# Kernel optimization log

Measured on AMD Instinct MI355X. Metric: run time of the kernel, lower is better.

The kernel has to match this reference:

```python
import jax, jax.numpy as jnp
import numpy as np

DIM = 1024
NUM_HEADS = 16
HEAD_DIM = DIM // NUM_HEADS
SCALE = HEAD_DIM ** -0.5


def setup_inputs() -> dict:
    key = jax.random.key(0)
    ks = jax.random.split(key, 13)
    B, Tq, Tk = 2, 1024, 4096
    s = DIM ** -0.5  # nn.Linear-like init scale
    inp = {
        'query': jax.random.normal(ks[0], (B, Tq, DIM), jnp.float32),
        'key': jax.random.normal(ks[1], (B, Tk, DIM), jnp.float32),
        'value': jax.random.normal(ks[2], (B, Tk, DIM), jnp.float32),
        'Wq': jax.random.normal(ks[3], (DIM, DIM), jnp.float32) * s,
        'bq': jnp.zeros((DIM,), jnp.float32),
        'Wk': jax.random.normal(ks[4], (DIM, DIM), jnp.float32) * s,
        'bk': jnp.zeros((DIM,), jnp.float32),
        'Wv': jax.random.normal(ks[5], (DIM, DIM), jnp.float32) * s,
        'bv': jnp.zeros((DIM,), jnp.float32),
        'Wo': jax.random.normal(ks[6], (DIM, DIM), jnp.float32) * s,
        'bo': jnp.zeros((DIM,), jnp.float32),
        'ln_gamma': jnp.ones((DIM,), jnp.float32),
        'ln_beta': jnp.zeros((DIM,), jnp.float32),
    }
    return inp


def _layer_norm(x, gamma, beta, eps=1e-5):
    mu = jnp.mean(x, axis=-1, keepdims=True)
    var = jnp.var(x, axis=-1, keepdims=True)
    return (x - mu) * jax.lax.rsqrt(var + eps) * gamma + beta


def reference(query, key, value, Wq, bq, Wk, bk, Wv, bv, Wo, bo, ln_gamma, ln_beta):
    B, Tq, D = query.shape
    Tk = key.shape[1]
    H, Hd = NUM_HEADS, HEAD_DIM
    # projections -> [B, H, T, Hd]
    q = (query @ Wq.T + bq).reshape(B, Tq, H, Hd).transpose(0, 2, 1, 3)
    k = (key @ Wk.T + bk).reshape(B, Tk, H, Hd).transpose(0, 2, 1, 3)
    v = (value @ Wv.T + bv).reshape(B, Tk, H, Hd).transpose(0, 2, 1, 3)
    scores = jnp.einsum('bhqd,bhkd->bhqk', q, k) * SCALE
    attn = jax.nn.softmax(scores, axis=-1)  # dropout is identity in eval
    out = jnp.einsum('bhqk,bhkd->bhqd', attn, v)
    out = out.transpose(0, 2, 1, 3).reshape(B, Tq, D)
    out = out @ Wo.T + bo
    out = _layer_norm(query + out, ln_gamma, ln_beta)
    return out, attn
```

## Files before the change

### kernel.cpp

```cpp
#include <hip/hip_runtime.h>
#include <hip/hip_bf16.h>

#define BATCH 2
#define TQ 1024
#define TK 4096
#define DIMSZ 1024
#define NH 16
#define HD 64
#define SCALE 0.125f

typedef __bf16 bf16x8 __attribute__((ext_vector_type(8)));
typedef float f32x4 __attribute__((ext_vector_type(4)));

static __device__ inline unsigned short f2bf(float x) {
  union { __bf16 h; unsigned short u; } v;
  v.h = (__bf16)x;
  return v.u;
}
static __device__ inline unsigned int pack2(float a, float b) {
  return (unsigned int)f2bf(a) | ((unsigned int)f2bf(b) << 16);
}

__global__ __launch_bounds__(256) void cast_all(
    const float* __restrict__ q, const float* __restrict__ k,
    const float* __restrict__ v, const float* __restrict__ wq,
    const float* __restrict__ wk, const float* __restrict__ wv,
    const float* __restrict__ wo, unsigned short* __restrict__ qo,
    unsigned short* __restrict__ ko, unsigned short* __restrict__ vo,
    unsigned short* __restrict__ wqo, unsigned short* __restrict__ wko,
    unsigned short* __restrict__ wvo, unsigned short* __restrict__ woo) {
  const float* src;
  unsigned short* dst;
  long n;
  switch (blockIdx.y) {
    case 0: src = q;  dst = qo;  n = (long)BATCH * TQ * DIMSZ; break;
    case 1: src = k;  dst = ko;  n = (long)BATCH * TK * DIMSZ; break;
    case 2: src = v;  dst = vo;  n = (long)BATCH * TK * DIMSZ; break;
    case 3: src = wq; dst = wqo; n = (long)DIMSZ * DIMSZ; break;
    case 4: src = wk; dst = wko; n = (long)DIMSZ * DIMSZ; break;
    case 5: src = wv; dst = wvo; n = (long)DIMSZ * DIMSZ; break;
    default: src = wo; dst = woo; n = (long)DIMSZ * DIMSZ; break;
  }
  const long stride = (long)gridDim.x * 256 * 8;
  for (long i = ((long)blockIdx.x * 256 + threadIdx.x) * 8; i < n; i += stride) {
    const float4 a = *(const float4*)&src[i];
    const float4 b = *(const float4*)&src[i + 4];
    uint4 o;
    o.x = pack2(a.x, a.y);
    o.y = pack2(a.z, a.w);
    o.z = pack2(b.x, b.y);
    o.w = pack2(b.z, b.w);
    *(uint4*)&dst[i] = o;
  }
}

template <bool OUT_BF16>
__global__ __launch_bounds__(256) void gemm_nt(
    const unsigned short* __restrict__ A, const unsigned short* __restrict__ B,
    const float* __restrict__ bias, void* __restrict__ Cout,
    int M, int N, int K) {
  __shared__ unsigned short As[128][40];
  __shared__ unsigned short Bs[128][40];
  const int t = threadIdx.x;
  const int lane = t & 63, wid = t >> 6;
  const int wm = wid >> 1, wn = wid & 1;
  const int l15 = lane & 15, l4 = lane >> 4;
  const int row0 = blockIdx.y * 128, col0 = blockIdx.x * 128;

  f32x4 acc[4][4];
#pragma unroll
  for (int i = 0; i < 4; i++)
#pragma unroll
    for (int j = 0; j < 4; j++) acc[i][j] = (f32x4){0.f, 0.f, 0.f, 0.f};

  for (int k0 = 0; k0 < K; k0 += 32) {
#pragma unroll
    for (int p = 0; p < 2; p++) {
      const int c = t + p * 256;
      const int r = c >> 2, kc = c & 3;
      *(uint4*)&As[r][kc * 8] =
          *(const uint4*)&A[(size_t)(row0 + r) * K + k0 + kc * 8];
      *(uint4*)&Bs[r][kc * 8] =
          *(const uint4*)&B[(size_t)(col0 + r) * K + k0 + kc * 8];
    }
    __syncthreads();
    bf16x8 av[4], bv[4];
#pragma unroll
    for (int f = 0; f < 4; f++) {
      av[f] = *(const bf16x8*)&As[wm * 64 + f * 16 + l15][l4 * 8];
      bv[f] = *(const bf16x8*)&Bs[wn * 64 + f * 16 + l15][l4 * 8];
    }
#pragma unroll
    for (int fm = 0; fm < 4; fm++)
#pragma unroll
      for (int fn = 0; fn < 4; fn++)
        acc[fm][fn] = __builtin_amdgcn_mfma_f32_16x16x32_bf16(
            av[fm], bv[fn], acc[fm][fn], 0, 0, 0);
    __syncthreads();
  }

#pragma unroll
  for (int fm = 0; fm < 4; fm++) {
#pragma unroll
    for (int i = 0; i < 4; i++) {
      const int rr = row0 + wm * 64 + fm * 16 + l4 * 4 + i;
#pragma unroll
      for (int fn = 0; fn < 4; fn++) {
        const int c = col0 + wn * 64 + fn * 16 + l15;
        const float val = acc[fm][fn][i] + bias[c];
        if (OUT_BF16)
          ((unsigned short*)Cout)[(size_t)rr * N + c] = f2bf(val);
        else
          ((float*)Cout)[(size_t)rr * N + c] = val;
      }
    }
  }
}

__global__ __launch_bounds__(256) void transpose_v(
    const unsigned short* __restrict__ vb, unsigned short* __restrict__ vT) {
  const int z = blockIdx.z, b = z >> 4, h = z & 15;
  const int k0 = blockIdx.x * 64;
  __shared__ unsigned short Ts[64][68];
  const int t = threadIdx.x;
  const int c4 = (t & 15) * 4, r = t >> 4;
#pragma unroll
  for (int p = 0; p < 4; p++) {
    const int rr = r + p * 16;
    *(uint2*)&Ts[rr][c4] =
        *(const uint2*)&vb[(size_t)(b * TK + k0 + rr) * DIMSZ + h * HD + c4];
  }
  __syncthreads();
#pragma unroll
  for (int p = 0; p < 4; p++) {
    const int c2 = t + p * 256;
    const int d = c2 >> 4, k4 = (c2 & 15) * 4;
    uint2 o;
    o.x = (unsigned int)Ts[k4][d] | ((unsigned int)Ts[k4 + 1][d] << 16);
    o.y = (unsigned int)Ts[k4 + 2][d] | ((unsigned int)Ts[k4 + 3][d] << 16);
    *(uint2*)&vT[(size_t)(z * HD + d) * TK + k0 + k4] = o;
  }
}

__global__ __launch_bounds__(256) void attn_fused(
    const unsigned short* __restrict__ qb, const unsigned short* __restrict__ kb,
    const unsigned short* __restrict__ vT, float* __restrict__ attn,
    unsigned short* __restrict__ aout) {
  const int dsp = blockIdx.x;
  const int orig = (dsp & 7) * 64 + (dsp >> 3);
  const int z = orig >> 4, mb = orig & 15;
  const int b = z >> 4, h = z & 15;
  const int m0 = mb * 64;

  __shared__ unsigned short Qs[64][72];
  __shared__ unsigned short Ks[128][72];
  __shared__ unsigned short Vs[64][140];
  __shared__ float Pf[64][132];
  __shared__ float partial[64][2];
  __shared__ float rinv[64];

  const int t = threadIdx.x;
  const int lane = t & 63, wid = t >> 6;
  const int wm = wid >> 1, wn = wid & 1;
  const int l15 = lane & 15, l4 = lane >> 4;

#pragma unroll
  for (int p = 0; p < 2; p++) {
    const int idx = t + p * 256;
    const int r = idx >> 3, kc = idx & 7;
    *(uint4*)&Qs[r][kc * 8] =
        *(const uint4*)&qb[(size_t)(b * TQ + m0 + r) * DIMSZ + h * HD + kc * 8];
  }
  __syncthreads();
  bf16x8 aq[2][2];
#pragma unroll
  for (int fm = 0; fm < 2; fm++)
#pragma unroll
    for (int ks = 0; ks < 2; ks++)
      aq[fm][ks] = *(const bf16x8*)&Qs[wm * 32 + fm * 16 + l15][ks * 32 + l4 * 8];

  float rsum[8];
#pragma unroll
  for (int r = 0; r < 8; r++) rsum[r] = 0.f;

  for (int kt = 0; kt < TK / 128; kt++) {
    __syncthreads();
#pragma unroll
    for (int p = 0; p < 4; p++) {
      const int idx = t + p * 256;
      const int r = idx >> 3, kc = idx & 7;
      *(uint4*)&Ks[r][kc * 8] = *(const uint4*)&kb[
          (size_t)(b * TK + kt * 128 + r) * DIMSZ + h * HD + kc * 8];
    }
    __syncthreads();
    bf16x8 bk_[4][2];
#pragma unroll
    for (int fn = 0; fn < 4; fn++)
#pragma unroll
      for (int ks = 0; ks < 2; ks++)
        bk_[fn][ks] =
            *(const bf16x8*)&Ks[wn * 64 + fn * 16 + l15][ks * 32 + l4 * 8];
    f32x4 acc_s[2][4];
#pragma unroll
    for (int i = 0; i < 2; i++)
#pragma unroll
      for (int j = 0; j < 4; j++) acc_s[i][j] = (f32x4){0.f, 0.f, 0.f, 0.f};
#pragma unroll
    for (int ks = 0; ks < 2; ks++)
#pragma unroll
      for (int fm = 0; fm < 2; fm++)
#pragma unroll
        for (int fn = 0; fn < 4; fn++)
          acc_s[fm][fn] = __builtin_amdgcn_mfma_f32_16x16x32_bf16(
              aq[fm][ks], bk_[fn][ks], acc_s[fm][fn], 0, 0, 0);
#pragma unroll
    for (int fm = 0; fm < 2; fm++)
#pragma unroll
      for (int i = 0; i < 4; i++) {
        float s = 0.f;
#pragma unroll
        for (int fn = 0; fn < 4; fn++) s += __expf(acc_s[fm][fn][i] * SCALE);
        rsum[fm * 4 + i] += s;
      }
  }
#pragma unroll
  for (int off = 1; off < 16; off <<= 1)
#pragma unroll
    for (int r = 0; r < 8; r++) rsum[r] += __shfl_xor(rsum[r], off);
  if (l15 == 0) {
#pragma unroll
    for (int fm = 0; fm < 2; fm++)
#pragma unroll
      for (int i = 0; i < 4; i++)
        partial[wm * 32 + fm * 16 + l4 * 4 + i][wn] = rsum[fm * 4 + i];
  }
  __syncthreads();
  if (t < 64) rinv[t] = 1.f / (partial[t][0] + partial[t][1]);

  f32x4 acc_o[4];
#pragma unroll
  for (int j = 0; j < 4; j++) acc_o[j] = (f32x4){0.f, 0.f, 0.f, 0.f};

  float* attn_z = attn + (size_t)z * TQ * TK;

  for (int kt = 0; kt < TK / 128; kt++) {
    __syncthreads();
#pragma unroll
    for (int p = 0; p < 4; p++) {
      const int idx = t + p * 256;
      const int r = idx >> 3, kc = idx & 7;
      *(uint4*)&Ks[r][kc * 8] = *(const uint4*)&kb[
          (size_t)(b * TK + kt * 128 + r) * DIMSZ + h * HD + kc * 8];
    }
#pragma unroll
    for (int p = 0; p < 4; p++) {
      const int idx = t + p * 256;
      const int d = idx >> 4, kc = idx & 15;
      *(uint4*)&Vs[d][kc * 8] =
          *(const uint4*)&vT[(size_t)(z * HD + d) * TK + kt * 128 + kc * 8];
    }
    __syncthreads();

    bf16x8 bk_[4][2];
#pragma unroll
    for (int fn = 0; fn < 4; fn++)
#pragma unroll
      for (int ks = 0; ks < 2; ks++)
        bk_[fn][ks] =
            *(const bf16x8*)&Ks[wn * 64 + fn * 16 + l15][ks * 32 + l4 * 8];
    f32x4 acc_s[2][4];
#pragma unroll
    for (int i = 0; i < 2; i++)
#pragma unroll
      for (int j = 0; j < 4; j++) acc_s[i][j] = (f32x4){0.f, 0.f, 0.f, 0.f};
#pragma unroll
    for (int ks = 0; ks < 2; ks++)
#pragma unroll
      for (int fm = 0; fm < 2; fm++)
#pragma unroll
        for (int fn = 0; fn < 4; fn++)
          acc_s[fm][fn] = __builtin_amdgcn_mfma_f32_16x16x32_bf16(
              aq[fm][ks], bk_[fn][ks], acc_s[fm][fn], 0, 0, 0);

#pragma unroll
    for (int fm = 0; fm < 2; fm++)
#pragma unroll
      for (int i = 0; i < 4; i++) {
        const int row = wm * 32 + fm * 16 + l4 * 4 + i;
        const float iv = rinv[row];
#pragma unroll
        for (int fn = 0; fn < 4; fn++) {
          const int col = wn * 64 + fn * 16 + l15;
          Pf[row][col] = __expf(acc_s[fm][fn][i] * SCALE) * iv;
        }
      }
    __syncthreads();

#pragma unroll
    for (int it = 0; it < 8; it++) {
      const int idx = t + it * 256;
      const int row = idx >> 5, c4 = idx & 31;
      const f32x4 v = *(const f32x4*)&Pf[row][c4 * 4];
      __builtin_nontemporal_store(
          v, (f32x4*)&attn_z[(size_t)(m0 + row) * TK + kt * 128 + c4 * 4]);
    }

#pragma unroll
    for (int ks2 = 0; ks2 < 4; ks2++) {
      const float* pr = &Pf[wid * 16 + l15][ks2 * 32 + l4 * 8];
      const float4 a0 = *(const float4*)pr;
      const float4 a1 = *(const float4*)(pr + 4);
      uint4 pk;
      pk.x = pack2(a0.x, a0.y);
      pk.y = pack2(a0.z, a0.w);
      pk.z = pack2(a1.x, a1.y);
      pk.w = pack2(a1.z, a1.w);
      const bf16x8 ap = *(const bf16x8*)&pk;
#pragma unroll
      for (int fn = 0; fn < 4; fn++) {
        const bf16x8 bvv =
            *(const bf16x8*)&Vs[fn * 16 + l15][ks2 * 32 + l4 * 8];
        acc_o[fn] = __builtin_amdgcn_mfma_f32_16x16x32_bf16(ap, bvv,
                                                            acc_o[fn], 0, 0, 0);
      }
    }
  }

#pragma unroll
  for (int fn = 0; fn < 4; fn++)
#pragma unroll
    for (int i = 0; i < 4; i++) {
      const int rr = m0 + wid * 16 + l4 * 4 + i;
      aout[(size_t)(b * TQ + rr) * DIMSZ + h * HD + fn * 16 + l15] =
          f2bf(acc_o[fn][i]);
    }
}

__global__ __launch_bounds__(256) void residual_ln(
    const float* __restrict__ q, const float* __restrict__ y,
    const float* __restrict__ gamma, const float* __restrict__ beta,
    float* __restrict__ out) {
  __shared__ float w1[4];
  __shared__ float w2[4];
  const size_t base = (size_t)blockIdx.x * DIMSZ;
  const int t = threadIdx.x;

  float x[4];
  float s = 0.f;
#pragma unroll
  for (int i = 0; i < 4; i++) {
    const int c = t + i * 256;
    x[i] = q[base + c] + y[base + c];
    s += x[i];
  }
#pragma unroll
  for (int off = 32; off; off >>= 1) s += __shfl_xor(s, off);
  if ((t & 63) == 0) w1[t >> 6] = s;
  __syncthreads();
  const float mean = (w1[0] + w1[1] + w1[2] + w1[3]) * (1.f / DIMSZ);

  float vs = 0.f;
#pragma unroll
  for (int i = 0; i < 4; i++) {
    const float d = x[i] - mean;
    vs += d * d;
  }
#pragma unroll
  for (int off = 32; off; off >>= 1) vs += __shfl_xor(vs, off);
  if ((t & 63) == 0) w2[t >> 6] = vs;
  __syncthreads();
  const float var = (w2[0] + w2[1] + w2[2] + w2[3]) * (1.f / DIMSZ);
  const float rstd = rsqrtf(var + 1e-5f);

#pragma unroll
  for (int i = 0; i < 4; i++) {
    const int c = t + i * 256;
    out[base + c] = (x[i] - mean) * rstd * gamma[c] + beta[c];
  }
}

extern "C" void kernel_launch(void* const* d_in, const int* in_sizes, int n_in,
                              void* d_out, int out_size, void* d_ws,
                              size_t ws_size, hipStream_t stream) {
  const float* query = (const float*)d_in[0];
  const float* key   = (const float*)d_in[1];
  const float* value = (const float*)d_in[2];
  const float* Wq = (const float*)d_in[3];
  const float* bq = (const float*)d_in[4];
  const float* Wk = (const float*)d_in[5];
  const float* bk = (const float*)d_in[6];
  const float* Wv = (const float*)d_in[7];
  const float* bv = (const float*)d_in[8];
  const float* Wo = (const float*)d_in[9];
  const float* bo = (const float*)d_in[10];
  const float* ln_gamma = (const float*)d_in[11];
  const float* ln_beta  = (const float*)d_in[12];

  float* out  = (float*)d_out;
  float* attn = out + (size_t)BATCH * TQ * DIMSZ;

  const size_t MQ = (size_t)BATCH * TQ * DIMSZ;
  const size_t MK = (size_t)BATCH * TK * DIMSZ;
  const size_t MM = (size_t)DIMSZ * DIMSZ;

  unsigned short* ws = (unsigned short*)d_ws;
  unsigned short* qbf = ws;
  unsigned short* kbf = qbf + MQ;
  unsigned short* vbf = kbf + MK;
  unsigned short* wqb = vbf + MK;
  unsigned short* wkb = wqb + MM;
  unsigned short* wvb = wkb + MM;
  unsigned short* wob = wvb + MM;
  unsigned short* qb  = wob + MM;
  unsigned short* kb  = qb + MQ;
  unsigned short* ab  = kb + MK;
  float* ybuf = (float*)(ab + MQ);

  unsigned short* vbp = kbf;
  unsigned short* vT  = vbf;

  const dim3 blk(256);

  cast_all<<<dim3(1024, 7), blk, 0, stream>>>(query, key, value, Wq, Wk, Wv,
                                              Wo, qbf, kbf, vbf, wqb, wkb,
                                              wvb, wob);

  gemm_nt<true><<<dim3(DIMSZ / 128, (BATCH * TQ) / 128), blk, 0, stream>>>(
      qbf, wqb, bq, qb, BATCH * TQ, DIMSZ, DIMSZ);
  gemm_nt<true><<<dim3(DIMSZ / 128, (BATCH * TK) / 128), blk, 0, stream>>>(
      kbf, wkb, bk, kb, BATCH * TK, DIMSZ, DIMSZ);
  gemm_nt<true><<<dim3(DIMSZ / 128, (BATCH * TK) / 128), blk, 0, stream>>>(
      vbf, wvb, bv, vbp, BATCH * TK, DIMSZ, DIMSZ);

  transpose_v<<<dim3(TK / 64, 1, BATCH * NH), blk, 0, stream>>>(vbp, vT);

  attn_fused<<<dim3(512), blk, 0, stream>>>(qb, kb, vT, attn, ab);

  gemm_nt<false><<<dim3(DIMSZ / 128, (BATCH * TQ) / 128), blk, 0, stream>>>(
      ab, wob, bo, ybuf, BATCH * TQ, DIMSZ, DIMSZ);

  residual_ln<<<dim3(BATCH * TQ), blk, 0, stream>>>(query, ybuf, ln_gamma,
                                                    ln_beta, out);
}
```

Baseline: 369.0 us.

## Halve attention query tile to 32 rows and double grid for occupancy

```diff
diff --git a/kernel.cpp b/kernel.cpp
--- a/kernel.cpp
+++ b/kernel.cpp
@@ -142,172 +142,139 @@
   }
 }
 
-__global__ __launch_bounds__(256) void attn_fused(
+__global__ __launch_bounds__(256, 4) void attn_fused(
     const unsigned short* __restrict__ qb, const unsigned short* __restrict__ kb,
     const unsigned short* __restrict__ vT, float* __restrict__ attn,
     unsigned short* __restrict__ aout) {
   const int dsp = blockIdx.x;
-  const int orig = (dsp & 7) * 64 + (dsp >> 3);
-  const int z = orig >> 4, mb = orig & 15;
+  const int orig = (dsp & 7) * 128 + (dsp >> 3);
+  const int z = orig >> 5, mb = orig & 31;
   const int b = z >> 4, h = z & 15;
-  const int m0 = mb * 64;
-
-  __shared__ unsigned short Qs[64][72];
-  __shared__ unsigned short Ks[128][72];
-  __shared__ unsigned short Vs[64][140];
-  __shared__ float Pf[64][132];
-  __shared__ float partial[64][2];
-  __shared__ float rinv[64];
+  const int m0 = mb * 32;
+
+  __shared__ unsigned short Qs[32][72];
+  __shared__ unsigned short Ks[64][72];
+  __shared__ unsigned short Vs[64][72];
+  __shared__ float Pf[32][68];
+  __shared__ float partial[32][2];
+  __shared__ float rinv[32];
 
   const int t = threadIdx.x;
   const int lane = t & 63, wid = t >> 6;
   const int wm = wid >> 1, wn = wid & 1;
   const int l15 = lane & 15, l4 = lane >> 4;
 
-#pragma unroll
-  for (int p = 0; p < 2; p++) {
-    const int idx = t + p * 256;
-    const int r = idx >> 3, kc = idx & 7;
+  const unsigned short* kb_z = kb + (size_t)b * TK * DIMSZ + h * HD;
+  const unsigned short* vT_z = vT + (size_t)z * HD * TK;
+
+  {
+    const int r = t >> 3, kc = t & 7;
     *(uint4*)&Qs[r][kc * 8] =
         *(const uint4*)&qb[(size_t)(b * TQ + m0 + r) * DIMSZ + h * HD + kc * 8];
   }
   __syncthreads();
-  bf16x8 aq[2][2];
-#pragma unroll
-  for (int fm = 0; fm < 2; fm++)
+  bf16x8 aq[2];
+#pragma unroll
+  for (int ks = 0; ks < 2; ks++)
+    aq[ks] = *(const bf16x8*)&Qs[wm * 16 + l15][ks * 32 + l4 * 8];
+
+  float rsum[4] = {0.f, 0.f, 0.f, 0.f};
+  for (int kt = 0; kt < TK / 64; kt++) {
+    bf16x8 bk_[2][2];
+#pragma unroll
+    for (int fn = 0; fn < 2; fn++)
+#pragma unroll
+      for (int ks = 0; ks < 2; ks++)
+        bk_[fn][ks] = *(const bf16x8*)&kb_z[
+            (size_t)(kt * 64 + wn * 32 + fn * 16 + l15) * DIMSZ + ks * 32 +
+            l4 * 8];
+    f32x4 acc_s[2];
+#pragma unroll
+    for (int j = 0; j < 2; j++) acc_s[j] = (f32x4){0.f, 0.f, 0.f, 0.f};
 #pragma unroll
     for (int ks = 0; ks < 2; ks++)
-      aq[fm][ks] = *(const bf16x8*)&Qs[wm * 32 + fm * 16 + l15][ks * 32 + l4 * 8];
-
-  float rsum[8];
-#pragma unroll
-  for (int r = 0; r < 8; r++) rsum[r] = 0.f;
-
-  for (int kt = 0; kt < TK / 128; kt++) {
+#pragma unroll
+      for (int fn = 0; fn < 2; fn++)
+        acc_s[fn] = __builtin_amdgcn_mfma_f32_16x16x32_bf16(
+            aq[ks], bk_[fn][ks], acc_s[fn], 0, 0, 0);
+#pragma unroll
+    for (int i = 0; i < 4; i++)
+      rsum[i] += __expf(acc_s[0][i] * SCALE) + __expf(acc_s[1][i] * SCALE);
+  }
+#pragma unroll
+  for (int off = 1; off < 16; off <<= 1)
+#pragma unroll
+    for (int i = 0; i < 4; i++) rsum[i] += __shfl_xor(rsum[i], off);
+  if (l15 == 0) {
+#pragma unroll
+    for (int i = 0; i < 4; i++)
+      partial[wm * 16 + l4 * 4 + i][wn] = rsum[i];
+  }
+  __syncthreads();
+  if (t < 32) rinv[t] = 1.f / (partial[t][0] + partial[t][1]);
+  __syncthreads();
+  float riv[4];
+#pragma unroll
+  for (int i = 0; i < 4; i++) riv[i] = rinv[wm * 16 + l4 * 4 + i];
+
+  f32x4 acc_o[2];
+#pragma unroll
+  for (int j = 0; j < 2; j++) acc_o[j] = (f32x4){0.f, 0.f, 0.f, 0.f};
+
+  float* attn_z = attn + (size_t)z * TQ * TK;
+
+  for (int kt = 0; kt < TK / 64; kt++) {
     __syncthreads();
 #pragma unroll
-    for (int p = 0; p < 4; p++) {
+    for (int p = 0; p < 2; p++) {
       const int idx = t + p * 256;
       const int r = idx >> 3, kc = idx & 7;
-      *(uint4*)&Ks[r][kc * 8] = *(const uint4*)&kb[
-          (size_t)(b * TK + kt * 128 + r) * DIMSZ + h * HD + kc * 8];
+      *(uint4*)&Ks[r][kc * 8] =
+          *(const uint4*)&kb_z[(size_t)(kt * 64 + r) * DIMSZ + kc * 8];
+      *(uint4*)&Vs[r][kc * 8] =
+          *(const uint4*)&vT_z[(size_t)r * TK + kt * 64 + kc * 8];
     }
     __syncthreads();
-    bf16x8 bk_[4][2];
-#pragma unroll
-    for (int fn = 0; fn < 4; fn++)
+
+    bf16x8 bk_[2][2];
+#pragma unroll
+    for (int fn = 0; fn < 2; fn++)
 #pragma unroll
       for (int ks = 0; ks < 2; ks++)
         bk_[fn][ks] =
-            *(const bf16x8*)&Ks[wn * 64 + fn * 16 + l15][ks * 32 + l4 * 8];
-    f32x4 acc_s[2][4];
-#pragma unroll
-    for (int i = 0; i < 2; i++)
-#pragma unroll
-      for (int j = 0; j < 4; j++) acc_s[i][j] = (f32x4){0.f, 0.f, 0.f, 0.f};
+            *(const bf16x8*)&Ks[wn * 32 + fn * 16 + l15][ks * 32 + l4 * 8];
+    f32x4 acc_s[2];
+#pragma unroll
+    for (int j = 0; j < 2; j++) acc_s[j] = (f32x4){0.f, 0.f, 0.f, 0.f};
 #pragma unroll
     for (int ks = 0; ks < 2; ks++)
 #pragma unroll
-      for (int fm = 0; fm < 2; fm++)
-#pragma unroll
-        for (int fn = 0; fn < 4; fn++)
-          acc_s[fm][fn] = __builtin_amdgcn_mfma_f32_16x16x32_bf16(
-              aq[fm][ks], bk_[fn][ks], acc_s[fm][fn], 0, 0, 0);
-#pragma unroll
-    for (int fm = 0; fm < 2; fm++)
+      for (int fn = 0; fn < 2; fn++)
+        acc_s[fn] = __builtin_amdgcn_mfma_f32_16x16x32_bf16(
+            aq[ks], bk_[fn][ks], acc_s[fn], 0, 0, 0);
+
+#pragma unroll
+    for (int fn = 0; fn < 2; fn++)
 #pragma unroll
       for (int i = 0; i < 4; i++) {
-        float s = 0.f;
-#pragma unroll
-        for (int fn = 0; fn < 4; fn++) s += __expf(acc_s[fm][fn][i] * SCALE);
-        rsum[fm * 4 + i] += s;
-      }
-  }
-#pragma unroll
-  for (int off = 1; off < 16; off <<= 1)
-#pragma unroll
-    for (int r = 0; r < 8; r++) rsum[r] += __shfl_xor(rsum[r], off);
-  if (l15 == 0) {
-#pragma unroll
-    for (int fm = 0; fm < 2; fm++)
-#pragma unroll
-      for (int i = 0; i < 4; i++)
-        partial[wm * 32 + fm * 16 + l4 * 4 + i][wn] = rsum[fm * 4 + i];
-  }
-  __syncthreads();
-  if (t < 64) rinv[t] = 1.f / (partial[t][0] + partial[t][1]);
-
-  f32x4 acc_o[4];
-#pragma unroll
-  for (int j = 0; j < 4; j++) acc_o[j] = (f32x4){0.f, 0.f, 0.f, 0.f};
-
-  float* attn_z = attn + (size_t)z * TQ * TK;
-
-  for (int kt = 0; kt < TK / 128; kt++) {
-    __syncthreads();
-#pragma unroll
-    for (int p = 0; p < 4; p++) {
-      const int idx = t + p * 256;
-      const int r = idx >> 3, kc = idx & 7;
-      *(uint4*)&Ks[r][kc * 8] = *(const uint4*)&kb[
-          (size_t)(b * TK + kt * 128 + r) * DIMSZ + h * HD + kc * 8];
-    }
-#pragma unroll
-    for (int p = 0; p < 4; p++) {
-      const int idx = t + p * 256;
-      const int d = idx >> 4, kc = idx & 15;
-      *(uint4*)&Vs[d][kc * 8] =
-          *(const uint4*)&vT[(size_t)(z * HD + d) * TK + kt * 128 + kc * 8];
-    }
-    __syncthreads();
-
-    bf16x8 bk_[4][2];
-#pragma unroll
-    for (int fn = 0; fn < 4; fn++)
-#pragma unroll
-      for (int ks = 0; ks < 2; ks++)
-        bk_[fn][ks] =
-            *(const bf16x8*)&Ks[wn * 64 + fn * 16 + l15][ks * 32 + l4 * 8];
-    f32x4 acc_s[2][4];
-#pragma unroll
-    for (int i = 0; i < 2; i++)
-#pragma unroll
-      for (int j = 0; j < 4; j++) acc_s[i][j] = (f32x4){0.f, 0.f, 0.f, 0.f};
-#pragma unroll
-    for (int ks = 0; ks < 2; ks++)
-#pragma unroll
-      for (int fm = 0; fm < 2; fm++)
-#pragma unroll
-        for (int fn = 0; fn < 4; fn++)
-          acc_s[fm][fn] = __builtin_amdgcn_mfma_f32_16x16x32_bf16(
-              aq[fm][ks], bk_[fn][ks], acc_s[fm][fn], 0, 0, 0);
-
-#pragma unroll
-    for (int fm = 0; fm < 2; fm++)
-#pragma unroll
-      for (int i = 0; i < 4; i++) {
-        const int row = wm * 32 + fm * 16 + l4 * 4 + i;
-        const float iv = rinv[row];
-#pragma unroll
-        for (int fn = 0; fn < 4; fn++) {
-          const int col = wn * 64 + fn * 16 + l15;
-          Pf[row][col] = __expf(acc_s[fm][fn][i] * SCALE) * iv;
-        }
+        const int row = wm * 16 + l4 * 4 + i;
+        const int col = wn * 32 + fn * 16 + l15;
+        Pf[row][col] = __expf(acc_s[fn][i] * SCALE) * riv[i];
       }
     __syncthreads();
 
 #pragma unroll
-    for (int it = 0; it < 8; it++) {
+    for (int it = 0; it < 2; it++) {
       const int idx = t + it * 256;
-      const int row = idx >> 5, c4 = idx & 31;
+      const int row = idx >> 4, c4 = idx & 15;
       const f32x4 v = *(const f32x4*)&Pf[row][c4 * 4];
       __builtin_nontemporal_store(
-          v, (f32x4*)&attn_z[(size_t)(m0 + row) * TK + kt * 128 + c4 * 4]);
-    }
-
-#pragma unroll
-    for (int ks2 = 0; ks2 < 4; ks2++) {
-      const float* pr = &Pf[wid * 16 + l15][ks2 * 32 + l4 * 8];
+          v, (f32x4*)&attn_z[(size_t)(m0 + row) * TK + kt * 64 + c4 * 4]);
+    }
+
+#pragma unroll
+    for (int ks2 = 0; ks2 < 2; ks2++) {
+      const float* pr = &Pf[wm * 16 + l15][ks2 * 32 + l4 * 8];
       const float4 a0 = *(const float4*)pr;
       const float4 a1 = *(const float4*)(pr + 4);
       uint4 pk;
@@ -317,9 +284,9 @@
       pk.w = pack2(a1.z, a1.w);
       const bf16x8 ap = *(const bf16x8*)&pk;
 #pragma unroll
-      for (int fn = 0; fn < 4; fn++) {
+      for (int fn = 0; fn < 2; fn++) {
         const bf16x8 bvv =
-            *(const bf16x8*)&Vs[fn * 16 + l15][ks2 * 32 + l4 * 8];
+            *(const bf16x8*)&Vs[wn * 32 + fn * 16 + l15][ks2 * 32 + l4 * 8];
         acc_o[fn] = __builtin_amdgcn_mfma_f32_16x16x32_bf16(ap, bvv,
                                                             acc_o[fn], 0, 0, 0);
       }
@@ -327,11 +294,11 @@
   }
 
 #pragma unroll
-  for (int fn = 0; fn < 4; fn++)
+  for (int fn = 0; fn < 2; fn++)
 #pragma unroll
     for (int i = 0; i < 4; i++) {
-      const int rr = m0 + wid * 16 + l4 * 4 + i;
-      aout[(size_t)(b * TQ + rr) * DIMSZ + h * HD + fn * 16 + l15] =
+      const int rr = m0 + wm * 16 + l4 * 4 + i;
+      aout[(size_t)(b * TQ + rr) * DIMSZ + h * HD + wn * 32 + fn * 16 + l15] =
           f2bf(acc_o[fn][i]);
     }
 }
@@ -434,7 +401,7 @@
 
   transpose_v<<<dim3(TK / 64, 1, BATCH * NH), blk, 0, stream>>>(vbp, vT);
 
-  attn_fused<<<dim3(512), blk, 0, stream>>>(qb, kb, vT, attn, ab);
+  attn_fused<<<dim3(1024), blk, 0, stream>>>(qb, kb, vT, attn, ab);
 
   gemm_nt<false><<<dim3(DIMSZ / 128, (BATCH * TQ) / 128), blk, 0, stream>>>(
       ab, wob, bo, ybuf, BATCH * TQ, DIMSZ, DIMSZ);
```

New measurement: 372.6 us. Within noise of the previous version (+1.0%).

## Use direct global-to-LDS loads in GEMM and merge QKV projections into one launch

Applied to the files above, without the earlier changes.

```diff
diff --git a/kernel.cpp b/kernel.cpp
--- a/kernel.cpp
+++ b/kernel.cpp
@@ -55,17 +55,18 @@
 }
 
 template <bool OUT_BF16>
-__global__ __launch_bounds__(256) void gemm_nt(
+static __device__ __forceinline__ void gemm_body(
     const unsigned short* __restrict__ A, const unsigned short* __restrict__ B,
-    const float* __restrict__ bias, void* __restrict__ Cout,
-    int M, int N, int K) {
-  __shared__ unsigned short As[128][40];
-  __shared__ unsigned short Bs[128][40];
+    const float* __restrict__ bias, void* __restrict__ Cout, int N, int K,
+    int row0, int col0) {
+  __shared__ unsigned short As[128][32];
+  __shared__ unsigned short Bs[128][32];
   const int t = threadIdx.x;
-  const int lane = t & 63, wid = t >> 6;
-  const int wm = wid >> 1, wn = wid & 1;
+  const int lane = t & 63, wv = t >> 6;
+  const int wm = wv >> 1, wn = wv & 1;
   const int l15 = lane & 15, l4 = lane >> 4;
-  const int row0 = blockIdx.y * 128, col0 = blockIdx.x * 128;
+  const int grow = lane >> 2;
+  const int gcol = (lane & 3) * 8;
 
   f32x4 acc[4][4];
 #pragma unroll
@@ -73,15 +74,23 @@
 #pragma unroll
     for (int j = 0; j < 4; j++) acc[i][j] = (f32x4){0.f, 0.f, 0.f, 0.f};
 
+  const unsigned short* pA = &A[(size_t)(row0 + wv * 32 + grow) * K + gcol];
+  const unsigned short* pB = &B[(size_t)(col0 + wv * 32 + grow) * K + gcol];
+
   for (int k0 = 0; k0 < K; k0 += 32) {
-#pragma unroll
-    for (int p = 0; p < 2; p++) {
-      const int c = t + p * 256;
-      const int r = c >> 2, kc = c & 3;
-      *(uint4*)&As[r][kc * 8] =
-          *(const uint4*)&A[(size_t)(row0 + r) * K + k0 + kc * 8];
-      *(uint4*)&Bs[r][kc * 8] =
-          *(const uint4*)&B[(size_t)(col0 + r) * K + k0 + kc * 8];
+    __syncthreads();
+#pragma unroll
+    for (int c = 0; c < 2; c++) {
+      __builtin_amdgcn_global_load_lds(
+          (const __attribute__((address_space(1))) unsigned int*)(
+              pA + (size_t)(c * 16) * K + k0),
+          (__attribute__((address_space(3))) unsigned int*)&As[wv * 32 + c * 16][0],
+          16, 0, 0);
+      __builtin_amdgcn_global_load_lds(
+          (const __attribute__((address_space(1))) unsigned int*)(
+              pB + (size_t)(c * 16) * K + k0),
+          (__attribute__((address_space(3))) unsigned int*)&Bs[wv * 32 + c * 16][0],
+          16, 0, 0);
     }
     __syncthreads();
     bf16x8 av[4], bv[4];
@@ -96,7 +105,6 @@
       for (int fn = 0; fn < 4; fn++)
         acc[fm][fn] = __builtin_amdgcn_mfma_f32_16x16x32_bf16(
             av[fm], bv[fn], acc[fm][fn], 0, 0, 0);
-    __syncthreads();
   }
 
 #pragma unroll
@@ -115,6 +123,35 @@
       }
     }
   }
+}
+
+__global__ __launch_bounds__(256) void proj_qkv(
+    const unsigned short* __restrict__ qbf, const unsigned short* __restrict__ kbf,
+    const unsigned short* __restrict__ vbf, const unsigned short* __restrict__ wqb,
+    const unsigned short* __restrict__ wkb, const unsigned short* __restrict__ wvb,
+    const float* __restrict__ bq, const float* __restrict__ bk,
+    const float* __restrict__ bv, unsigned short* __restrict__ qb,
+    unsigned short* __restrict__ kb, unsigned short* __restrict__ vbp) {
+  const int y = blockIdx.y;
+  const unsigned short *A, *B;
+  const float* bias;
+  unsigned short* C;
+  int row0;
+  if (y < 64) {
+    A = kbf; B = wkb; bias = bk; C = kb; row0 = y * 128;
+  } else if (y < 128) {
+    A = vbf; B = wvb; bias = bv; C = vbp; row0 = (y - 64) * 128;
+  } else {
+    A = qbf; B = wqb; bias = bq; C = qb; row0 = (y - 128) * 128;
+  }
+  gemm_body<true>(A, B, bias, C, DIMSZ, DIMSZ, row0, blockIdx.x * 128);
+}
+
+__global__ __launch_bounds__(256) void proj_o(
+    const unsigned short* __restrict__ A, const unsigned short* __restrict__ B,
+    const float* __restrict__ bias, float* __restrict__ C) {
+  gemm_body<false>(A, B, bias, C, DIMSZ, DIMSZ, blockIdx.y * 128,
+                   blockIdx.x * 128);
 }
 
 __global__ __launch_bounds__(256) void transpose_v(
@@ -413,11 +450,10 @@
   unsigned short* wob = wvb + MM;
   unsigned short* qb  = wob + MM;
   unsigned short* kb  = qb + MQ;
-  unsigned short* ab  = kb + MK;
-  float* ybuf = (float*)(ab + MQ);
-
-  unsigned short* vbp = kbf;
-  unsigned short* vT  = vbf;
+  unsigned short* vbp = kb + MK;
+  unsigned short* vT = kbf;
+  unsigned short* ab = qbf;
+  float* ybuf = (float*)vbf;
 
   const dim3 blk(256);
 
@@ -425,19 +461,15 @@
                                               Wo, qbf, kbf, vbf, wqb, wkb,
                                               wvb, wob);
 
-  gemm_nt<true><<<dim3(DIMSZ / 128, (BATCH * TQ) / 128), blk, 0, stream>>>(
-      qbf, wqb, bq, qb, BATCH * TQ, DIMSZ, DIMSZ);
-  gemm_nt<true><<<dim3(DIMSZ / 128, (BATCH * TK) / 128), blk, 0, stream>>>(
-      kbf, wkb, bk, kb, BATCH * TK, DIMSZ, DIMSZ);
-  gemm_nt<true><<<dim3(DIMSZ / 128, (BATCH * TK) / 128), blk, 0, stream>>>(
-      vbf, wvb, bv, vbp, BATCH * TK, DIMSZ, DIMSZ);
+  proj_qkv<<<dim3(DIMSZ / 128, 144), blk, 0, stream>>>(
+      qbf, kbf, vbf, wqb, wkb, wvb, bq, bk, bv, qb, kb, vbp);
 
   transpose_v<<<dim3(TK / 64, 1, BATCH * NH), blk, 0, stream>>>(vbp, vT);
 
   attn_fused<<<dim3(512), blk, 0, stream>>>(qb, kb, vT, attn, ab);
 
-  gemm_nt<false><<<dim3(DIMSZ / 128, (BATCH * TQ) / 128), blk, 0, stream>>>(
-      ab, wob, bo, ybuf, BATCH * TQ, DIMSZ, DIMSZ);
+  proj_o<<<dim3(DIMSZ / 128, (BATCH * TQ) / 128), blk, 0, stream>>>(ab, wob,
+                                                                    bo, ybuf);
 
   residual_ln<<<dim3(BATCH * TQ), blk, 0, stream>>>(query, ybuf, ln_gamma,
                                                     ln_beta, out);
```

After: 337.3 us. 8.6% less time.
